# Optimization experiments

Hardware: AMD Instinct MI355X
Metric: run time of the kernel (lower is better)

The kernel has to match this reference:

```python
import jax, jax.numpy as jnp
import numpy as np

T, WS, SHIFT, HEADS, DIM = 5, (8, 8), (4, 4), 6, 192
HEAD_DIM = DIM // HEADS
SCALE = HEAD_DIM ** -0.5
MLP_HID = 4 * DIM
TABLE_LEN = (T * 2 * WS[0] - 1) * (2 * WS[1] - 1)


def _rel_index():
    # exact replica of WindowAttention.__init__ index construction (t,h,w coords)
    ct, ch, cw = np.arange(T), np.arange(WS[0]), np.arange(WS[1])
    coords = np.stack(np.meshgrid(ct, ch, cw, indexing='ij')).reshape(3, -1)
    rel = (coords[:, :, None] - coords[:, None, :]).transpose(1, 2, 0).astype(np.int64)
    rel[:, :, 0] += WS[0] - 1
    rel[:, :, 1] += WS[1] - 1
    rel[:, :, 0] *= 2 * WS[1] - 1
    return jnp.asarray(rel.sum(-1))  # (N, N)


def _attn_mask(H, W):
    # standard shifted-window mask on (H,W); identical across T, so tile (T,T)
    img = np.zeros((H, W), np.float32)
    cnt = 0
    for hs in (slice(0, -WS[0]), slice(-WS[0], -SHIFT[0]), slice(-SHIFT[0], None)):
        for ws_ in (slice(0, -WS[1]), slice(-WS[1], -SHIFT[1]), slice(-SHIFT[1], None)):
            img[hs, ws_] = cnt
            cnt += 1
    img = img.reshape(H // WS[0], WS[0], W // WS[1], WS[1]).transpose(0, 2, 1, 3)
    img = img.reshape(-1, WS[0] * WS[1])  # (nW, Wh*Ww)
    m = img[:, None, :] - img[:, :, None]
    m = np.where(m != 0, -100.0, 0.0).astype(np.float32)
    return jnp.asarray(np.tile(m, (1, T, T)))  # (nW, T*Wh*Ww, T*Wh*Ww)


def _win_part(x, ws):
    B, t, H, W, C = x.shape
    x = x.reshape(B, t, H // ws[0], ws[0], W // ws[1], ws[1], C)
    return x.transpose(0, 2, 4, 1, 3, 5, 6).reshape(-1, t * ws[0] * ws[1], C)


def _win_rev(w, ws, H, W, t, B):
    x = w.reshape(B, H // ws[0], W // ws[1], t, ws[0], ws[1], -1)
    return x.transpose(0, 3, 1, 4, 2, 5, 6).reshape(B, t, H, W, -1)


def _ln(x, g, b):
    mu = x.mean(-1, keepdims=True)
    var = ((x - mu) ** 2).mean(-1, keepdims=True)
    return (x - mu) * jax.lax.rsqrt(var + 1e-5) * g + b


def _forward(x, ln1_g, ln1_b, qkv_w, qkv_b, rel_bias_table, proj_w, proj_b,
             ln2_g, ln2_b, fc1_w, fc1_b, fc2_w, fc2_b, H, W):
    B, L, C = x.shape
    shortcut = x
    h = _ln(x, ln1_g, ln1_b)
    qkv = h @ qkv_w.T + qkv_b                                   # (B, L, 3C)
    qkv = qkv.reshape(B, T, H, W, 3 * C)
    qkv = jnp.roll(qkv, (-SHIFT[0], -SHIFT[1]), axis=(2, 3))
    qkv = _win_part(qkv, WS)                                    # (B_, N, 3C)
    B_, N, _ = qkv.shape
    qkv = qkv.reshape(B_, N, 3, HEADS, HEAD_DIM).transpose(2, 0, 3, 1, 4)
    q, k, v = qkv[0], qkv[1], qkv[2]
    attn = jnp.einsum('bhnd,bhmd->bhnm', q * SCALE, k)          # (B_, H, N, N)
    bias = rel_bias_table[_rel_index()].transpose(2, 0, 1)      # (heads, N, N)
    attn = attn + bias[None]
    mask = _attn_mask(H, W)                                     # (nW, N, N)
    nW = mask.shape[0]
    attn = attn.reshape(B_ // nW, nW, HEADS, N, N) + mask[None, :, None]
    attn = jax.nn.softmax(attn.reshape(B_, HEADS, N, N), axis=-1)
    out = jnp.einsum('bhnm,bhmd->bhnd', attn, v)
    out = out.transpose(0, 2, 1, 3).reshape(B_, N, C)
    out = out @ proj_w.T + proj_b
    out = _win_rev(out, WS, H, W, T, B)
    out = jnp.roll(out, (SHIFT[0], SHIFT[1]), axis=(2, 3)).reshape(B, L, C)
    x = shortcut + out
    h = _ln(x, ln2_g, ln2_b)
    h = jax.nn.gelu(h @ fc1_w.T + fc1_b, approximate=False) @ fc2_w.T + fc2_b
    return x + h


def setup_inputs() -> dict:
    key = jax.random.key(0)
    ks = jax.random.split(key, 8)
    B, Himg, Wimg = 2, 64, 64
    L = T * Himg * Wimg
    s = 0.02
    return {
        'x': jax.random.normal(ks[0], (B, L, DIM), jnp.float32),
        'ln1_g': jnp.ones((DIM,), jnp.float32),
        'ln1_b': jnp.zeros((DIM,), jnp.float32),
        'qkv_w': jax.random.normal(ks[1], (3 * DIM, DIM), jnp.float32) * s,
        'qkv_b': jnp.zeros((3 * DIM,), jnp.float32),
        'rel_bias_table': jax.random.normal(ks[2], (TABLE_LEN, HEADS), jnp.float32) * s,
        'proj_w': jax.random.normal(ks[3], (DIM, DIM), jnp.float32) * s,
        'proj_b': jnp.zeros((DIM,), jnp.float32),
        'ln2_g': jnp.ones((DIM,), jnp.float32),
        'ln2_b': jnp.zeros((DIM,), jnp.float32),
        'fc1_w': jax.random.normal(ks[4], (MLP_HID, DIM), jnp.float32) * s,
        'fc1_b': jnp.zeros((MLP_HID,), jnp.float32),
        'fc2_w': jax.random.normal(ks[5], (DIM, MLP_HID), jnp.float32) * s,
        'fc2_b': jnp.zeros((DIM,), jnp.float32),
        'H': Himg,
        'W': Wimg,
    }


def reference(x, ln1_g, ln1_b, qkv_w, qkv_b, rel_bias_table, proj_w, proj_b,
              ln2_g, ln2_b, fc1_w, fc1_b, fc2_w, fc2_b, H, W):
    return _forward(x, ln1_g, ln1_b, qkv_w, qkv_b, rel_bias_table, proj_w, proj_b,
                    ln2_g, ln2_b, fc1_w, fc1_b, fc2_w, fc2_b, H, W)
```

## Files before the change

kernel.cpp:

```cpp
#include <hip/hip_runtime.h>
#include <math.h>

typedef unsigned short u16;
typedef unsigned int u32;
typedef short bf16x8 __attribute__((ext_vector_type(8)));
typedef float f32x4 __attribute__((ext_vector_type(4)));
typedef _Float16 f16x4 __attribute__((ext_vector_type(4)));

#define TT 5
#define HEADS 6
#define HD 32
#define DIM 192
#define NWIN 320
#define LTOK (TT*64*64)
#define BATCH 2
#define MROWS (BATCH*LTOK)
#define QSCALE 0.17677669529663687f

__device__ __forceinline__ u16 f2bf(float f) {
    u32 u = __float_as_uint(f);
    u32 r = (u + 0x7FFFu + ((u >> 16) & 1u)) >> 16;
    return (u16)r;
}
__device__ __forceinline__ float bflo(u32 u) { return __uint_as_float(u << 16); }
__device__ __forceinline__ float bfhi(u32 u) { return __uint_as_float(u & 0xFFFF0000u); }
__device__ __forceinline__ u32 pkh(float a, float b) {
    auto h = __builtin_amdgcn_cvt_pkrtz(a, b);
    return __builtin_bit_cast(u32, h);
}

__global__ __launch_bounds__(256) void cvt_kernel(
    const float* __restrict__ in, u16* __restrict__ out, int n)
{
    int i = blockIdx.x * 256 + threadIdx.x;
    if (i < n) out[i] = f2bf(in[i]);
}

__global__ __launch_bounds__(256) void ln_kernel(
    const float* __restrict__ x, const float* __restrict__ g,
    const float* __restrict__ b, u16* __restrict__ out)
{
    int tok  = blockIdx.x * 4 + (threadIdx.x >> 6);
    int lane = threadIdx.x & 63;
    const float* xr = x + (size_t)tok * DIM;
    float v0 = xr[lane], v1 = xr[lane + 64], v2 = xr[lane + 128];
    float s = v0 + v1 + v2;
    #pragma unroll
    for (int off = 32; off; off >>= 1) s += __shfl_xor(s, off, 64);
    float mu = s * (1.0f / 192.0f);
    float d0 = v0 - mu, d1 = v1 - mu, d2 = v2 - mu;
    float vs = d0 * d0 + d1 * d1 + d2 * d2;
    #pragma unroll
    for (int off = 32; off; off >>= 1) vs += __shfl_xor(vs, off, 64);
    float rstd = rsqrtf(vs * (1.0f / 192.0f) + 1e-5f);
    u16* orow = out + (size_t)tok * DIM;
    orow[lane]       = f2bf(d0 * rstd * g[lane]       + b[lane]);
    orow[lane + 64]  = f2bf(d1 * rstd * g[lane + 64]  + b[lane + 64]);
    orow[lane + 128] = f2bf(d2 * rstd * g[lane + 128] + b[lane + 128]);
}

template<int EPI>
__global__ __launch_bounds__(256) void mfma_gemm(
    const u16* __restrict__ A, const u16* __restrict__ W,
    const float* __restrict__ bias, void* __restrict__ outp,
    const float* __restrict__ xin, int N, int K)
{
    __shared__ u16 As[128 * 64];
    __shared__ u16 Bs[64 * 64];
    const int tid  = threadIdx.x;
    const int lane = tid & 63, wv = tid >> 6;
    const int ln16 = lane & 15, quad = lane >> 4;
    const int bn = blockIdx.x, bm = blockIdx.y;

    const int srow = lane >> 3;
    const int sxor = (lane & 7) ^ srow;
    const int acol = sxor * 8;

    f32x4 acc[2][4] = {};

    for (int k0 = 0; k0 < K; k0 += 64) {
        __syncthreads();
        #pragma unroll
        for (int a = 0; a < 4; ++a) {
            const u16* g = A + (size_t)(bm * 128 + a * 32 + wv * 8 + srow) * K + k0 + acol;
            __builtin_amdgcn_global_load_lds(
                (const __attribute__((address_space(1))) u32*)g,
                (__attribute__((address_space(3))) u32*)((char*)As + a * 4096 + wv * 1024),
                16, 0, 0);
        }
        #pragma unroll
        for (int bb = 0; bb < 2; ++bb) {
            const u16* g = W + (size_t)(bn * 64 + bb * 32 + wv * 8 + srow) * K + k0 + acol;
            __builtin_amdgcn_global_load_lds(
                (const __attribute__((address_space(1))) u32*)g,
                (__attribute__((address_space(3))) u32*)((char*)Bs + bb * 4096 + wv * 1024),
                16, 0, 0);
        }
        __syncthreads();
        #pragma unroll
        for (int s = 0; s < 2; ++s) {
            bf16x8 af[2], bf[4];
            #pragma unroll
            for (int i = 0; i < 2; ++i) {
                int r = wv * 32 + i * 16 + ln16;
                int slot = (s * 4 + quad) ^ (r & 7);
                af[i] = *(const bf16x8*)((const char*)As + r * 128 + slot * 16);
            }
            #pragma unroll
            for (int j = 0; j < 4; ++j) {
                int r = j * 16 + ln16;
                int slot = (s * 4 + quad) ^ (r & 7);
                bf[j] = *(const bf16x8*)((const char*)Bs + r * 128 + slot * 16);
            }
            #pragma unroll
            for (int i = 0; i < 2; ++i)
                #pragma unroll
                for (int j = 0; j < 4; ++j)
                    acc[i][j] = __builtin_amdgcn_mfma_f32_16x16x32_bf16(
                        af[i], bf[j], acc[i][j], 0, 0, 0);
        }
    }

    #pragma unroll
    for (int i = 0; i < 2; ++i) {
        int gr0 = bm * 128 + wv * 32 + i * 16 + quad * 4;
        #pragma unroll
        for (int j = 0; j < 4; ++j) {
            int gc = bn * 64 + j * 16 + ln16;
            float bv = bias[gc];
            #pragma unroll
            for (int rr = 0; rr < 4; ++rr) {
                int gr = gr0 + rr;
                float val = acc[i][j][rr] + bv;
                if (EPI == 0) {
                    ((u16*)outp)[(size_t)gr * N + gc] = f2bf(val);
                } else if (EPI == 1) {
                    float gl = val * 0.5f * (1.0f + erff(val * 0.70710678118654752f));
                    ((u16*)outp)[(size_t)gr * N + gc] = f2bf(gl);
                } else if (EPI == 2) {
                    int b_ = gr / NWIN, n = gr - b_ * NWIN;
                    int b = b_ >> 6, hb = (b_ >> 3) & 7, wb = b_ & 7;
                    int t = n >> 6, hi = (n >> 3) & 7, wj = n & 7;
                    int hs = (hb * 8 + hi + 4) & 63;
                    int wsrc = (wb * 8 + wj + 4) & 63;
                    size_t dst = ((size_t)b * LTOK + t * 4096 + hs * 64 + wsrc) * DIM + gc;
                    ((float*)outp)[dst] = xin[dst] + val;
                } else {
                    ((float*)outp)[(size_t)gr * N + gc] += val;
                }
            }
        }
    }
}

__global__ __launch_bounds__(320) void attn_kernel(
    const u16* __restrict__ qkv, const float* __restrict__ table,
    u16* __restrict__ attout)
{
    const int head = blockIdx.x % HEADS;
    const int b_   = blockIdx.x / HEADS;
    const int b = b_ >> 6, hb = (b_ >> 3) & 7, wb = b_ & 7;
    const int tid = threadIdx.x;
    const int lane = tid & 63, wv = tid >> 6;
    const int ln16 = lane & 15, quad = lane >> 4;

    __shared__ u16 Ks[320 * 40];
    __shared__ u16 Vt[32 * 328];
    __shared__ u16 meta[320];
    __shared__ float tbl[188];

    {
        int n = tid;
        int t1 = n >> 6, r1 = (n >> 3) & 7, c1 = n & 7;
        int h1 = hb * 8 + r1, w1 = wb * 8 + c1;
        int l1 = t1 * 4096 + ((h1 + 4) & 63) * 64 + ((w1 + 4) & 63);
        const u16* src = qkv + ((size_t)b * LTOK + l1) * (3 * DIM) + head * HD;
        const uint4* k4 = (const uint4*)(src + DIM);
        #pragma unroll
        for (int i = 0; i < 4; ++i)
            *(uint4*)(Ks + n * 40 + i * 8) = k4[i];
        const uint4* v4 = (const uint4*)(src + 2 * DIM);
        #pragma unroll
        for (int i = 0; i < 4; ++i) {
            uint4 u = v4[i];
            u32 ws[4] = {u.x, u.y, u.z, u.w};
            #pragma unroll
            for (int j = 0; j < 4; ++j) {
                u32 hb2 = pkh(bflo(ws[j]), bfhi(ws[j]));
                int d = i * 8 + j * 2;
                Vt[d * 328 + n]       = (u16)(hb2 & 0xFFFF);
                Vt[(d + 1) * 328 + n] = (u16)(hb2 >> 16);
            }
        }
        int off = (7 - t1) * 15 + 7 - r1 - c1;
        int rh = h1 < 56 ? 0 : (h1 < 60 ? 1 : 2);
        int rw = w1 < 56 ? 0 : (w1 < 60 ? 1 : 2);
        meta[n] = (u16)(off | ((rh * 3 + rw) << 8));
        if (n < 187) tbl[n] = table[n * HEADS + head];
    }

    bf16x8 qf[4];
    int basen[4], myreg[4];
    #pragma unroll
    for (int qt = 0; qt < 4; ++qt) {
        int nq = wv * 64 + qt * 16 + ln16;
        int t1 = nq >> 6, r1 = (nq >> 3) & 7, c1 = nq & 7;
        int h1 = hb * 8 + r1, w1 = wb * 8 + c1;
        int l1 = t1 * 4096 + ((h1 + 4) & 63) * 64 + ((w1 + 4) & 63);
        qf[qt] = *(const bf16x8*)(qkv + ((size_t)b * LTOK + l1) * (3 * DIM)
                                  + head * HD + quad * 8);
        basen[qt] = t1 * 15 + r1 + c1;
        int rh = h1 < 56 ? 0 : (h1 < 60 ? 1 : 2);
        int rw = w1 < 56 ? 0 : (w1 < 60 ? 1 : 2);
        myreg[qt] = rh * 3 + rw;
    }

    __syncthreads();

    f32x4 o[4][2] = {};
    float m_[4] = {-1e30f, -1e30f, -1e30f, -1e30f};
    float l_[4] = {};
    const f32x4 zero = {};

    #pragma unroll 1
    for (int c = 0; c < 10; ++c) {
        int kb = c * 32;
        bf16x8 af0 = *(const bf16x8*)(Ks + (kb + ln16) * 40 + quad * 8);
        bf16x8 af1 = *(const bf16x8*)(Ks + (kb + 16 + ln16) * 40 + quad * 8);
        f16x4 va[2][2];
        #pragma unroll
        for (int dt = 0; dt < 2; ++dt)
            #pragma unroll
            for (int kt = 0; kt < 2; ++kt)
                va[dt][kt] = *(const f16x4*)(Vt + (dt * 16 + ln16) * 328
                                             + kb + kt * 16 + quad * 4);
        ushort4 m4a = *(const ushort4*)(meta + kb + quad * 4);
        ushort4 m4b = *(const ushort4*)(meta + kb + 16 + quad * 4);
        u16 mta[4] = {m4a.x, m4a.y, m4a.z, m4a.w};
        u16 mtb[4] = {m4b.x, m4b.y, m4b.z, m4b.w};

        #pragma unroll
        for (int qt = 0; qt < 4; ++qt) {
            f32x4 s0 = __builtin_amdgcn_mfma_f32_16x16x32_bf16(af0, qf[qt], zero, 0, 0, 0);
            f32x4 s1 = __builtin_amdgcn_mfma_f32_16x16x32_bf16(af1, qf[qt], zero, 0, 0, 0);
            float p[8];
            #pragma unroll
            for (int r = 0; r < 4; ++r) {
                int ma = mta[r], mb = mtb[r];
                float va0 = fmaf(s0[r], QSCALE, tbl[basen[qt] + (ma & 0xFF)]);
                float vb0 = fmaf(s1[r], QSCALE, tbl[basen[qt] + (mb & 0xFF)]);
                p[r]     = va0 + (((ma >> 8) == myreg[qt]) ? 0.0f : -100.0f);
                p[4 + r] = vb0 + (((mb >> 8) == myreg[qt]) ? 0.0f : -100.0f);
            }
            float cm = p[0];
            #pragma unroll
            for (int j = 1; j < 8; ++j) cm = fmaxf(cm, p[j]);
            cm = fmaxf(cm, __shfl_xor(cm, 16, 64));
            cm = fmaxf(cm, __shfl_xor(cm, 32, 64));
            float mn = fmaxf(m_[qt], cm);
            float rs = __expf(m_[qt] - mn);
            m_[qt] = mn;
            float ls = 0.0f;
            #pragma unroll
            for (int j = 0; j < 8; ++j) { p[j] = __expf(p[j] - mn); ls += p[j]; }
            l_[qt] = l_[qt] * rs + ls;
            #pragma unroll
            for (int dt = 0; dt < 2; ++dt) {
                o[qt][dt][0] *= rs; o[qt][dt][1] *= rs;
                o[qt][dt][2] *= rs; o[qt][dt][3] *= rs;
            }
            uint2 pk0 = { pkh(p[0], p[1]), pkh(p[2], p[3]) };
            uint2 pk1 = { pkh(p[4], p[5]), pkh(p[6], p[7]) };
            f16x4 pf0 = __builtin_bit_cast(f16x4, pk0);
            f16x4 pf1 = __builtin_bit_cast(f16x4, pk1);
            #pragma unroll
            for (int dt = 0; dt < 2; ++dt) {
                o[qt][dt] = __builtin_amdgcn_mfma_f32_16x16x16f16(va[dt][0], pf0, o[qt][dt], 0, 0, 0);
                o[qt][dt] = __builtin_amdgcn_mfma_f32_16x16x16f16(va[dt][1], pf1, o[qt][dt], 0, 0, 0);
            }
        }
    }

    #pragma unroll
    for (int qt = 0; qt < 4; ++qt) {
        float lt = l_[qt];
        lt += __shfl_xor(lt, 16, 64);
        lt += __shfl_xor(lt, 32, 64);
        float inv = 1.0f / lt;
        int nq = wv * 64 + qt * 16 + ln16;
        u16* dst = attout + ((size_t)(b_ * NWIN + nq)) * DIM + head * HD + quad * 4;
        #pragma unroll
        for (int dt = 0; dt < 2; ++dt) {
            u32 w0 = (u32)f2bf(o[qt][dt][0] * inv) | ((u32)f2bf(o[qt][dt][1] * inv) << 16);
            u32 w1 = (u32)f2bf(o[qt][dt][2] * inv) | ((u32)f2bf(o[qt][dt][3] * inv) << 16);
            uint2 st = {w0, w1};
            *(uint2*)(dst + dt * 16) = st;
        }
    }
}

extern "C" void kernel_launch(void* const* d_in, const int* in_sizes, int n_in,
                              void* d_out, int out_size, void* d_ws, size_t ws_size,
                              hipStream_t stream)
{
    (void)in_sizes; (void)n_in; (void)out_size; (void)ws_size;
    const float* x      = (const float*)d_in[0];
    const float* ln1_g  = (const float*)d_in[1];
    const float* ln1_b  = (const float*)d_in[2];
    const float* qkv_w  = (const float*)d_in[3];
    const float* qkv_b  = (const float*)d_in[4];
    const float* table  = (const float*)d_in[5];
    const float* proj_w = (const float*)d_in[6];
    const float* proj_b = (const float*)d_in[7];
    const float* ln2_g  = (const float*)d_in[8];
    const float* ln2_b  = (const float*)d_in[9];
    const float* fc1_w  = (const float*)d_in[10];
    const float* fc1_b  = (const float*)d_in[11];
    const float* fc2_w  = (const float*)d_in[12];
    const float* fc2_b  = (const float*)d_in[13];
    float* out = (float*)d_out;

    u16* wsu     = (u16*)d_ws;
    u16* h_buf   = wsu;
    u16* qkv_buf = wsu + (size_t)MROWS * DIM;
    u16* att_buf = wsu + (size_t)MROWS * (4 * DIM);
    u16* fc1_buf = wsu + (size_t)MROWS * DIM;
    u16* wq = wsu + (size_t)MROWS * (5 * DIM);
    u16* wp = wq + 3 * DIM * DIM;
    u16* w1 = wp + DIM * DIM;
    u16* w2 = w1 + 4 * DIM * DIM;

    cvt_kernel<<<3 * DIM * DIM / 256, 256, 0, stream>>>(qkv_w, wq, 3 * DIM * DIM);
    cvt_kernel<<<DIM * DIM / 256, 256, 0, stream>>>(proj_w, wp, DIM * DIM);
    cvt_kernel<<<4 * DIM * DIM / 256, 256, 0, stream>>>(fc1_w, w1, 4 * DIM * DIM);
    cvt_kernel<<<4 * DIM * DIM / 256, 256, 0, stream>>>(fc2_w, w2, 4 * DIM * DIM);

    ln_kernel<<<MROWS / 4, 256, 0, stream>>>(x, ln1_g, ln1_b, h_buf);
    mfma_gemm<0><<<dim3(3 * DIM / 64, MROWS / 128), 256, 0, stream>>>(
        h_buf, wq, qkv_b, qkv_buf, nullptr, 3 * DIM, DIM);
    attn_kernel<<<128 * HEADS, 320, 0, stream>>>(qkv_buf, table, att_buf);
    mfma_gemm<2><<<dim3(DIM / 64, MROWS / 128), 256, 0, stream>>>(
        att_buf, wp, proj_b, out, x, DIM, DIM);
    ln_kernel<<<MROWS / 4, 256, 0, stream>>>(out, ln2_g, ln2_b, h_buf);
    mfma_gemm<1><<<dim3(4 * DIM / 64, MROWS / 128), 256, 0, stream>>>(
        h_buf, w1, fc1_b, fc1_buf, nullptr, 4 * DIM, DIM);
    mfma_gemm<3><<<dim3(DIM / 64, MROWS / 128), 256, 0, stream>>>(
        fc1_buf, w2, fc2_b, out, nullptr, DIM, 4 * DIM);
}
```

Baseline: 293.5 us.

## Use exp2 softmax with lazy rescaling, fold mask into bias, merge weight casts

The attention softmax now works in base 2: the scale and bias table are pre-multiplied by log2(e) and the raw v_exp_f32 instruction replaces __expf. Masked positions get a -30000 bias through a select, so the separate add of -100 goes away. The running max and the rescaling of the accumulators are now updated only when some lane's new max exceeds the old one by a threshold, which skips the cross-lane shuffles and rescale multiplies most of the time. Alongside this, the four weight-conversion launches are merged into one kernel, the chunk loop is unrolled by 2, and attn_kernel gets an occupancy hint through launch bounds. The lazy max lets exponentials reach up to 2^12 before rescaling, which costs some headroom against fp16 overflow in P, and the stronger mask changes results slightly relative to the -100 reference.

```diff
diff --git a/kernel.cpp b/kernel.cpp
--- a/kernel.cpp
+++ b/kernel.cpp
@@ -16,6 +16,9 @@
 #define BATCH 2
 #define MROWS (BATCH*LTOK)
 #define QSCALE 0.17677669529663687f
+#define LOG2E 1.4426950408889634f
+#define QSCALE2 (QSCALE * LOG2E)
+#define RTHR 12.0f
 
 __device__ __forceinline__ u16 f2bf(float f) {
     u32 u = __float_as_uint(f);
@@ -28,12 +31,25 @@
     auto h = __builtin_amdgcn_cvt_pkrtz(a, b);
     return __builtin_bit_cast(u32, h);
 }
-
-__global__ __launch_bounds__(256) void cvt_kernel(
-    const float* __restrict__ in, u16* __restrict__ out, int n)
+#if __has_builtin(__builtin_amdgcn_exp2f)
+__device__ __forceinline__ float ex2(float x) { return __builtin_amdgcn_exp2f(x); }
+#else
+__device__ __forceinline__ float ex2(float x) {
+    float r; asm("v_exp_f32 %0, %1" : "=v"(r) : "v"(x)); return r;
+}
+#endif
+
+__global__ __launch_bounds__(256) void cvt4_kernel(
+    const float* __restrict__ a, const float* __restrict__ b,
+    const float* __restrict__ c, const float* __restrict__ d,
+    u16* __restrict__ oa, u16* __restrict__ ob,
+    u16* __restrict__ oc, u16* __restrict__ od)
 {
     int i = blockIdx.x * 256 + threadIdx.x;
-    if (i < n) out[i] = f2bf(in[i]);
+    if (i < 110592)       oa[i]          = f2bf(a[i]);
+    else if (i < 147456)  ob[i - 110592] = f2bf(b[i - 110592]);
+    else if (i < 294912)  oc[i - 147456] = f2bf(c[i - 147456]);
+    else                  od[i - 294912] = f2bf(d[i - 294912]);
 }
 
 __global__ __launch_bounds__(256) void ln_kernel(
@@ -153,7 +169,7 @@
     }
 }
 
-__global__ __launch_bounds__(320) void attn_kernel(
+__global__ __launch_bounds__(320, 4) void attn_kernel(
     const u16* __restrict__ qkv, const float* __restrict__ table,
     u16* __restrict__ attout)
 {
@@ -196,7 +212,7 @@
         int rh = h1 < 56 ? 0 : (h1 < 60 ? 1 : 2);
         int rw = w1 < 56 ? 0 : (w1 < 60 ? 1 : 2);
         meta[n] = (u16)(off | ((rh * 3 + rw) << 8));
-        if (n < 187) tbl[n] = table[n * HEADS + head];
+        if (n < 187) tbl[n] = table[n * HEADS + head] * LOG2E;
     }
 
     bf16x8 qf[4];
@@ -222,7 +238,7 @@
     float l_[4] = {};
     const f32x4 zero = {};
 
-    #pragma unroll 1
+    #pragma unroll 2
     for (int c = 0; c < 10; ++c) {
         int kb = c * 32;
         bf16x8 af0 = *(const bf16x8*)(Ks + (kb + ln16) * 40 + quad * 8);
@@ -247,28 +263,31 @@
             #pragma unroll
             for (int r = 0; r < 4; ++r) {
                 int ma = mta[r], mb = mtb[r];
-                float va0 = fmaf(s0[r], QSCALE, tbl[basen[qt] + (ma & 0xFF)]);
-                float vb0 = fmaf(s1[r], QSCALE, tbl[basen[qt] + (mb & 0xFF)]);
-                p[r]     = va0 + (((ma >> 8) == myreg[qt]) ? 0.0f : -100.0f);
-                p[4 + r] = vb0 + (((mb >> 8) == myreg[qt]) ? 0.0f : -100.0f);
-            }
-            float cm = p[0];
-            #pragma unroll
-            for (int j = 1; j < 8; ++j) cm = fmaxf(cm, p[j]);
-            cm = fmaxf(cm, __shfl_xor(cm, 16, 64));
-            cm = fmaxf(cm, __shfl_xor(cm, 32, 64));
-            float mn = fmaxf(m_[qt], cm);
-            float rs = __expf(m_[qt] - mn);
-            m_[qt] = mn;
+                float ba = ((ma >> 8) == myreg[qt]) ? tbl[basen[qt] + (ma & 0xFF)] : -30000.0f;
+                float bb = ((mb >> 8) == myreg[qt]) ? tbl[basen[qt] + (mb & 0xFF)] : -30000.0f;
+                p[r]     = fmaf(s0[r], QSCALE2, ba);
+                p[4 + r] = fmaf(s1[r], QSCALE2, bb);
+            }
+            float pm = p[0];
+            #pragma unroll
+            for (int j = 1; j < 8; ++j) pm = fmaxf(pm, p[j]);
+            if (__any(pm > m_[qt] + RTHR)) {
+                float cm = fmaxf(pm, __shfl_xor(pm, 16, 64));
+                cm = fmaxf(cm, __shfl_xor(cm, 32, 64));
+                float mn = fmaxf(m_[qt], cm);
+                float rs = ex2(m_[qt] - mn);
+                m_[qt] = mn;
+                l_[qt] *= rs;
+                #pragma unroll
+                for (int dt = 0; dt < 2; ++dt) {
+                    o[qt][dt][0] *= rs; o[qt][dt][1] *= rs;
+                    o[qt][dt][2] *= rs; o[qt][dt][3] *= rs;
+                }
+            }
             float ls = 0.0f;
             #pragma unroll
-            for (int j = 0; j < 8; ++j) { p[j] = __expf(p[j] - mn); ls += p[j]; }
-            l_[qt] = l_[qt] * rs + ls;
-            #pragma unroll
-            for (int dt = 0; dt < 2; ++dt) {
-                o[qt][dt][0] *= rs; o[qt][dt][1] *= rs;
-                o[qt][dt][2] *= rs; o[qt][dt][3] *= rs;
-            }
+            for (int j = 0; j < 8; ++j) { p[j] = ex2(p[j] - m_[qt]); ls += p[j]; }
+            l_[qt] += ls;
             uint2 pk0 = { pkh(p[0], p[1]), pkh(p[2], p[3]) };
             uint2 pk1 = { pkh(p[4], p[5]), pkh(p[6], p[7]) };
             f16x4 pf0 = __builtin_bit_cast(f16x4, pk0);
@@ -330,10 +349,8 @@
     u16* w1 = wp + DIM * DIM;
     u16* w2 = w1 + 4 * DIM * DIM;
 
-    cvt_kernel<<<3 * DIM * DIM / 256, 256, 0, stream>>>(qkv_w, wq, 3 * DIM * DIM);
-    cvt_kernel<<<DIM * DIM / 256, 256, 0, stream>>>(proj_w, wp, DIM * DIM);
-    cvt_kernel<<<4 * DIM * DIM / 256, 256, 0, stream>>>(fc1_w, w1, 4 * DIM * DIM);
-    cvt_kernel<<<4 * DIM * DIM / 256, 256, 0, stream>>>(fc2_w, w2, 4 * DIM * DIM);
+    cvt4_kernel<<<(12 * DIM * DIM) / 256, 256, 0, stream>>>(
+        qkv_w, proj_w, fc1_w, fc2_w, wq, wp, w1, w2);
 
     ln_kernel<<<MROWS / 4, 256, 0, stream>>>(x, ln1_g, ln1_b, h_buf);
     mfma_gemm<0><<<dim3(3 * DIM / 64, MROWS / 128), 256, 0, stream>>>(
```

Result: slower. 310.5 us (+5.8%).
